# Performance work log

Measured on AMD Instinct MI355X. Metric: run time of the kernel, lower is better.

The kernel has to match this reference:

```python
import jax, jax.numpy as jnp
import numpy as np

NUM_CODES = 8192
CODE_DIM = 64
DECAY = 0.99
EPS = 1e-05


def setup_inputs() -> dict:
    key = jax.random.key(0)
    k1, k2 = jax.random.split(key)
    z = jax.random.normal(k1, (8, CODE_DIM, 64, 64), dtype=jnp.float32)
    embed = jax.random.normal(k2, (NUM_CODES, CODE_DIM), dtype=jnp.float32)
    embed = embed / jnp.linalg.norm(embed, axis=1, keepdims=True)  # F.normalize(dim=1)
    cluster_size = jnp.zeros((NUM_CODES,), dtype=jnp.float32)
    embed_avg = embed * 1.0
    return {"z": z, "embed": embed, "cluster_size": cluster_size, "embed_avg": embed_avg}


def reference(z, embed, cluster_size, embed_avg):
    B, C, H, W = z.shape
    # (B,C,H,W) -> (N, C), N = B*H*W
    flat = jnp.transpose(z, (0, 2, 3, 1)).reshape(-1, C)
    x2 = jnp.sum(flat * flat, axis=1, keepdims=True)
    e2 = jnp.sum(embed * embed, axis=1)[None, :]
    logits = x2 + e2 - 2.0 * (flat @ embed.T)
    codes = jnp.argmin(logits, axis=1)
    # gather nearest code vectors, restore (B,C,H,W)
    z_q = jnp.transpose(embed[codes].reshape(B, H, W, C), (0, 3, 1, 2))
    # EMA update (training path; equivalent to one-hot matmul via segment sums)
    cs_batch = jax.ops.segment_sum(jnp.ones_like(codes, dtype=flat.dtype), codes, num_segments=NUM_CODES)
    embed_sum = jax.ops.segment_sum(flat, codes, num_segments=NUM_CODES)
    new_cluster_size = cluster_size * DECAY + cs_batch * (1.0 - DECAY)
    new_embed_avg = embed_avg * DECAY + embed_sum * (1.0 - DECAY)
    n = jnp.sum(new_cluster_size)
    cs_smoothed = (new_cluster_size + EPS) / (n + NUM_CODES * EPS) * n
    new_embed = new_embed_avg / cs_smoothed[:, None]
    new_embed = new_embed / jnp.linalg.norm(new_embed, axis=1, keepdims=True)
    return z_q, codes.reshape(B, H, W), new_embed, new_cluster_size, new_embed_avg
```

## Files before the change

kernel.cpp:

```cpp
#include <hip/hip_runtime.h>
#include <math.h>
#include <float.h>

#define NPTS   32768
#define NCODES 8192
#define D      64
#define HWSZ   4096
#define KSPLIT 8
#define NSTAGE 16

#define DECAY_F 0.99f
#define OMD_F   ((float)(1.0 - 0.99))
#define EPS_F   1e-5f

typedef __attribute__((ext_vector_type(8)))  short bf16x8;
typedef __attribute__((ext_vector_type(8)))  unsigned short us8;
typedef __attribute__((ext_vector_type(4)))  float f32x4;
typedef __attribute__((ext_vector_type(16))) float f32x16;

#define ZQ_OFF    0
#define CODES_OFF 2097152
#define NE_OFF    2129920
#define NCS_OFF   2654208
#define NEA_OFF   2662400

#define WS_PSUM   0
#define WS_ME2    64
#define WS_HIST   8256
#define WS_BOFF   16448
#define WS_BOFF2  24640
#define WS_CODES  32832
#define WS_ORDER  65600
#define WS_PMG    98368
#define WS_EBI    1146944
#define WS_ZROW   1409088

__device__ __forceinline__ unsigned short f2bf(float x) {
    unsigned int u = __float_as_uint(x);
    unsigned int r = (u + 0x7fffu + ((u >> 16) & 1u)) >> 16;
    return (unsigned short)r;
}
__device__ __forceinline__ float bf2f(unsigned short b) {
    return __uint_as_float(((unsigned int)b) << 16);
}

__global__ __launch_bounds__(256) void k_prep_e(
    const float* __restrict__ embed,
    unsigned short* __restrict__ ebi,
    float* __restrict__ me2, int* __restrict__ hist)
{
    const int tid = threadIdx.x;
    const int c = blockIdx.x * 32 + (tid >> 3);
    const int s = tid & 7;
    const float4 v0 = *(const float4*)(embed + (size_t)c * D + s * 8);
    const float4 v1 = *(const float4*)(embed + (size_t)c * D + s * 8 + 4);
    float x[8] = {v0.x, v0.y, v0.z, v0.w, v1.x, v1.y, v1.z, v1.w};
    float s2 = 0.f;
#pragma unroll
    for (int j = 0; j < 8; ++j) s2 += x[j] * x[j];
    s2 += __shfl_xor(s2, 1);
    s2 += __shfl_xor(s2, 2);
    s2 += __shfl_xor(s2, 4);
    us8 p0, p1;
#pragma unroll
    for (int j = 0; j < 8; ++j) {
        unsigned short a = f2bf(x[j]);
        float r = x[j] - bf2f(a);
        p0[j] = a; p1[j] = f2bf(r);
    }
    const int sg = c >> 6, ci = c & 63;
    unsigned short* tile = ebi + (size_t)sg * 8192;
    *(us8*)(tile + s * 512 + ci * 8) = p0;
    *(us8*)(tile + 4096 + s * 512 + ci * 8) = p1;
    if (s == 0) {
        me2[c] = -0.5f * s2;
        hist[c] = 0;
    }
}

#define MFMA32 __builtin_amdgcn_mfma_f32_32x32x16_bf16

#define TOP2(nt, g, gi) { \
    bool c1 = (g) > b1m[nt]; \
    bool c2 = (g) > b2m[nt]; \
    b2m[nt] = c1 ? b1m[nt] : (c2 ? (g) : b2m[nt]); \
    b2g[nt] = c1 ? b1g[nt] : (c2 ? (gi) : b2g[nt]); \
    b1m[nt] = c1 ? (g) : b1m[nt]; \
    b1g[nt] = c1 ? (gi) : b1g[nt]; }

#define GMAX8(a, o) fmaxf(fmaxf(fmaxf(fmaxf(a[o+0], a[o+1]), a[o+2]), \
                                fmaxf(fmaxf(a[o+3], a[o+4]), a[o+5])), \
                          fmaxf(a[o+6], a[o+7]))

__global__ __launch_bounds__(256, 3) void k_argmin_mfma(
    const float* __restrict__ z,
    const unsigned short* __restrict__ ebi,
    float* __restrict__ pmg)
{
    __shared__ __align__(16) char ets[2 * 16384];

    const int tid = threadIdx.x;
    const int l = tid & 63;
    const int w = tid >> 6;
    const int l31 = l & 31;
    const int hi = l >> 5;
    const int split = blockIdx.x >> 7;
    const int pgrp  = blockIdx.x & 127;
    const int n0    = pgrp * 256;
    const int b     = n0 >> 12;
    const int hw0   = n0 & 4095;
    const int ptw   = n0 + w * 64;

    const char* ebase = (const char*)ebi;
#define ISSUE_STAGE(sg_, buf_) { \
    const char* gsrc_ = ebase + (size_t)(sg_) * 16384; \
    _Pragma("unroll") \
    for (int i_ = 0; i_ < 4; ++i_) { \
        __builtin_amdgcn_global_load_lds( \
            (const __attribute__((address_space(1))) void*)(gsrc_ + i_ * 4096 + w * 1024 + l * 16), \
            (__attribute__((address_space(3))) void*)(ets + (buf_) * 16384 + i_ * 4096 + w * 1024), \
            16, 0, 0); \
    } }

    ISSUE_STAGE(split * NSTAGE, 0)

    const float* zb = z + (size_t)b * D * HWSZ;
    us8 zf[2][2][4];
#pragma unroll
    for (int nt = 0; nt < 2; ++nt) {
        const int hwp = hw0 + w * 64 + nt * 32 + l31;
#pragma unroll
        for (int kc = 0; kc < 4; ++kc) {
            us8 p0, p1;
#pragma unroll
            for (int j = 0; j < 8; ++j) {
                float x = zb[(size_t)(kc * 16 + hi * 8 + j) * HWSZ + hwp];
                unsigned short a = f2bf(x);
                float r = x - bf2f(a);
                p0[j] = a; p1[j] = f2bf(r);
            }
            zf[nt][0][kc] = p0; zf[nt][1][kc] = p1;
        }
    }

    f32x16 zerov;
#pragma unroll
    for (int r = 0; r < 16; ++r) zerov[r] = 0.f;

    __syncthreads();

    float b1m[2] = {-FLT_MAX, -FLT_MAX}, b2m[2] = {-FLT_MAX, -FLT_MAX};
    int   b1g[2] = {0, 0},               b2g[2] = {0, 0};

    for (int stg = 0; stg < NSTAGE; ++stg) {
        const int sg = split * NSTAGE + stg;
        if (stg) {
            asm volatile("s_waitcnt vmcnt(0)" ::: "memory");
            __builtin_amdgcn_s_barrier();
            __builtin_amdgcn_sched_barrier(0);
        }
        if (stg + 1 < NSTAGE) ISSUE_STAGE(sg + 1, (stg + 1) & 1)

        const char* bt = ets + (stg & 1) * 16384;

        f32x16 accA0, accA1, accB0, accB1;
#pragma unroll
        for (int kc = 0; kc < 4; ++kc) {
            const size_t offc0 = (size_t)(kc * 2 + hi) * 1024 + (size_t)l31 * 16;
            const size_t offc1 = offc0 + 32 * 16;
            bf16x8 ea0c0 = *(const bf16x8*)(bt + offc0);
            bf16x8 ea1c0 = *(const bf16x8*)(bt + 8192 + offc0);
            bf16x8 ea0c1 = *(const bf16x8*)(bt + offc1);
            bf16x8 ea1c1 = *(const bf16x8*)(bt + 8192 + offc1);
            if (kc == 0) {
                accA0 = MFMA32(ea1c0, (bf16x8)zf[0][0][0], zerov, 0, 0, 0);
                accB0 = MFMA32(ea1c1, (bf16x8)zf[0][0][0], zerov, 0, 0, 0);
                accA1 = MFMA32(ea1c0, (bf16x8)zf[1][0][0], zerov, 0, 0, 0);
                accB1 = MFMA32(ea1c1, (bf16x8)zf[1][0][0], zerov, 0, 0, 0);
            } else {
                accA0 = MFMA32(ea1c0, (bf16x8)zf[0][0][kc], accA0, 0, 0, 0);
                accB0 = MFMA32(ea1c1, (bf16x8)zf[0][0][kc], accB0, 0, 0, 0);
                accA1 = MFMA32(ea1c0, (bf16x8)zf[1][0][kc], accA1, 0, 0, 0);
                accB1 = MFMA32(ea1c1, (bf16x8)zf[1][0][kc], accB1, 0, 0, 0);
            }
            accA0 = MFMA32(ea0c0, (bf16x8)zf[0][1][kc], accA0, 0, 0, 0);
            accB0 = MFMA32(ea0c1, (bf16x8)zf[0][1][kc], accB0, 0, 0, 0);
            accA1 = MFMA32(ea0c0, (bf16x8)zf[1][1][kc], accA1, 0, 0, 0);
            accB1 = MFMA32(ea0c1, (bf16x8)zf[1][1][kc], accB1, 0, 0, 0);
            accA0 = MFMA32(ea0c0, (bf16x8)zf[0][0][kc], accA0, 0, 0, 0);
            accB0 = MFMA32(ea0c1, (bf16x8)zf[0][0][kc], accB0, 0, 0, 0);
            accA1 = MFMA32(ea0c0, (bf16x8)zf[1][0][kc], accA1, 0, 0, 0);
            accB1 = MFMA32(ea0c1, (bf16x8)zf[1][0][kc], accB1, 0, 0, 0);
        }

        {
            const int gb0 = sg * 8 + hi;
            const int gb1 = sg * 8 + 4 + hi;
            float a00 = GMAX8(accA0, 0), a01 = GMAX8(accA0, 8);
            float a10 = GMAX8(accA1, 0), a11 = GMAX8(accA1, 8);
            float b00 = GMAX8(accB0, 0), b01 = GMAX8(accB0, 8);
            float b10 = GMAX8(accB1, 0), b11 = GMAX8(accB1, 8);
            TOP2(0, a00, gb0)
            TOP2(0, a01, gb0 + 2)
            TOP2(1, a10, gb0)
            TOP2(1, a11, gb0 + 2)
            TOP2(0, b00, gb1)
            TOP2(0, b01, gb1 + 2)
            TOP2(1, b10, gb1)
            TOP2(1, b11, gb1 + 2)
        }
    }

#pragma unroll
    for (int nt = 0; nt < 2; ++nt) {
        float o1 = __shfl_xor(b1m[nt], 32); int o1g = __shfl_xor(b1g[nt], 32);
        float o2 = __shfl_xor(b2m[nt], 32); int o2g = __shfl_xor(b2g[nt], 32);
        float n1m, n2m; int n1g, n2g;
        if (o1 > b1m[nt]) {
            n1m = o1; n1g = o1g;
            if (b1m[nt] >= o2) { n2m = b1m[nt]; n2g = b1g[nt]; } else { n2m = o2; n2g = o2g; }
        } else {
            n1m = b1m[nt]; n1g = b1g[nt];
            if (o1 >= b2m[nt]) { n2m = o1; n2g = o1g; } else { n2m = b2m[nt]; n2g = b2g[nt]; }
        }
        b1m[nt] = n1m; b1g[nt] = n1g; b2m[nt] = n2m; b2g[nt] = n2g;
    }
    if (l < 32) {
#pragma unroll
        for (int nt = 0; nt < 2; ++nt) {
            int pt = ptw + nt * 32 + l31;
            float4 v = {b1m[nt], __int_as_float(b1g[nt]), b2m[nt], __int_as_float(b2g[nt])};
            *(float4*)(pmg + ((size_t)split * NPTS + pt) * 4) = v;
        }
    }
}

__device__ __forceinline__ int grp_code(int g, int s) {
    int base = (g >> 3) * 64 + ((g >> 2) & 1) * 32 + ((g >> 1) & 1) * 16 + (g & 1) * 4;
    return base + (s & 3) + ((s >> 2) & 1) * 8;
}

__global__ __launch_bounds__(256) void k_refine(
    const float* __restrict__ z, const float* __restrict__ embed,
    const float* __restrict__ me2, const float* __restrict__ pmg,
    int* __restrict__ codes_i, float* __restrict__ out_codes,
    float* __restrict__ zq, int* __restrict__ hist, float* __restrict__ zrow)
{
    __shared__ float  xs[64 * 32];
    __shared__ float4 smg[256];
    __shared__ float  sbm[256];
    __shared__ int    sbi[256];
    const int tid = threadIdx.x;
    const int pi = tid & 31, s = tid >> 5;
    const int n0 = blockIdx.x * 32;
    const int b = n0 >> 12, hw0 = n0 & 4095;
    const int n = n0 + pi;

    {
        float4 v = ((const float4*)pmg)[(size_t)(tid & 7) * NPTS + n0 + (tid >> 3)];
        smg[(tid & 7) * 32 + (tid >> 3)] = v;
    }
    const float* zb = z + (size_t)b * D * HWSZ + hw0;
#pragma unroll
    for (int i = 0; i < 8; ++i) {
        int c = s * 8 + i;
        xs[c * 32 + pi] = zb[(size_t)c * HWSZ + pi];
    }
    __syncthreads();
    float x[64];
#pragma unroll
    for (int c = 0; c < 64; ++c) x[c] = xs[c * 32 + pi];

    float t1 = -FLT_MAX, t2 = -FLT_MAX; int g1 = 0, g2 = 0;
#pragma unroll
    for (int j = 0; j < 8; ++j) {
        float4 v = smg[j * 32 + pi];
        float m1 = v.x; int a1 = __float_as_int(v.y);
        float m2 = v.z; int a2 = __float_as_int(v.w);
        if (m1 > t1) { t2 = t1; g2 = g1; t1 = m1; g1 = a1; }
        else if (m1 > t2) { t2 = m1; g2 = a1; }
        if (m2 > t1) { t2 = t1; g2 = g1; t1 = m2; g1 = a2; }
        else if (m2 > t2) { t2 = m2; g2 = a2; }
    }

    float bm = -FLT_MAX; int bi = 0x7fffffff;
#pragma unroll
    for (int cset = 0; cset < 2; ++cset) {
        const int ci = grp_code(cset ? g2 : g1, s);
        const float4* er = (const float4*)(embed + (size_t)ci * D);
        float d0 = 0.f, d1 = 0.f, d2 = 0.f, d3 = 0.f;
#pragma unroll
        for (int q = 0; q < 16; ++q) {
            float4 e4 = er[q];
            d0 = fmaf(x[4 * q + 0], e4.x, d0);
            d1 = fmaf(x[4 * q + 1], e4.y, d1);
            d2 = fmaf(x[4 * q + 2], e4.z, d2);
            d3 = fmaf(x[4 * q + 3], e4.w, d3);
        }
        float m = ((d0 + d1) + (d2 + d3)) + me2[ci];
        if (m > bm || (m == bm && ci < bi)) { bm = m; bi = ci; }
    }
    sbm[tid] = bm; sbi[tid] = bi;
    __syncthreads();

    if (s == 0) {
        float B = sbm[pi]; int I = sbi[pi];
#pragma unroll
        for (int t = 1; t < 8; ++t) {
            float mm = sbm[t * 32 + pi]; int ii = sbi[t * 32 + pi];
            if (mm > B || (mm == B && ii < I)) { B = mm; I = ii; }
        }
        codes_i[n] = I;
        out_codes[n] = (float)I;
        atomicAdd(&hist[I], 1);
        sbi[pi] = I;
    }
    __syncthreads();
    {
        const int I = sbi[pi];
        const float* err = embed + (size_t)I * D;
        const float4 e0 = *(const float4*)(err + s * 8);
        const float4 e1 = *(const float4*)(err + s * 8 + 4);
        float ev[8] = {e0.x, e0.y, e0.z, e0.w, e1.x, e1.y, e1.z, e1.w};
        size_t zoff = (size_t)b * D * HWSZ + hw0 + pi;
#pragma unroll
        for (int j = 0; j < 8; ++j)
            zq[zoff + (size_t)(s * 8 + j) * HWSZ] = ev[j];
    }
    {
        float4 a4 = {x[s * 8 + 0], x[s * 8 + 1], x[s * 8 + 2], x[s * 8 + 3]};
        float4 b4 = {x[s * 8 + 4], x[s * 8 + 5], x[s * 8 + 6], x[s * 8 + 7]};
        *(float4*)(zrow + (size_t)n * 64 + s * 8) = a4;
        *(float4*)(zrow + (size_t)n * 64 + s * 8 + 4) = b4;
    }
}

__global__ __launch_bounds__(1024) void k_scan(
    const int* __restrict__ hist, const float* __restrict__ cs_in,
    int* __restrict__ binoff, int* __restrict__ binoff2, float* __restrict__ psum)
{
    __shared__ int wtot[16];
    __shared__ int wbase[16];
    __shared__ float csw[16];
    const int tid = threadIdx.x;
    const int lane = tid & 63, w = tid >> 6;
    int v[8]; int s = 0;
    float cz = 0.f;
#pragma unroll
    for (int i = 0; i < 8; ++i) {
        v[i] = hist[tid * 8 + i];
        s += v[i];
        cz += cs_in[tid * 8 + i];
    }
    int inc = s;
#pragma unroll
    for (int off = 1; off < 64; off <<= 1) {
        int t = __shfl_up(inc, off);
        if (lane >= off) inc += t;
    }
    cz += __shfl_xor(cz, 32); cz += __shfl_xor(cz, 16); cz += __shfl_xor(cz, 8);
    cz += __shfl_xor(cz, 4);  cz += __shfl_xor(cz, 2);  cz += __shfl_xor(cz, 1);
    if (lane == 63) wtot[w] = inc;
    if (lane == 0)  csw[w] = cz;
    __syncthreads();
    if (tid == 0) {
        int a = 0;
        float S = 0.f;
#pragma unroll
        for (int i = 0; i < 16; ++i) { int t = wtot[i]; wbase[i] = a; a += t; S += csw[i]; }
        psum[0] = S;
    }
    __syncthreads();
    int excl = wbase[w] + (inc - s);
#pragma unroll
    for (int i = 0; i < 8; ++i) {
        binoff[tid * 8 + i] = excl;
        binoff2[tid * 8 + i] = excl;
        excl += v[i];
    }
}

__global__ void k_reorder(const int* __restrict__ codes_i,
                          int* __restrict__ binoff2, int* __restrict__ order)
{
    int n = blockIdx.x * 256 + threadIdx.x;
    int c = codes_i[n];
    int r = atomicAdd(&binoff2[c], 1);
    order[r] = n;
}

__global__ __launch_bounds__(256) void k_accum(
    const int* __restrict__ hist, const int* __restrict__ binoff,
    const int* __restrict__ order, const float* __restrict__ zrow,
    const float* __restrict__ cs, const float* __restrict__ eavg,
    const float* __restrict__ psum,
    float* __restrict__ out_ncs, float* __restrict__ out_nea, float* __restrict__ out_ne)
{
    int k = blockIdx.x * 4 + (threadIdx.x >> 6);
    int lane = threadIdx.x & 63;
    int cnt = hist[k], base = binoff[k];
    float acc = 0.f;
    for (int i = 0; i < cnt; ++i) {
        int p = order[base + i];
        acc += zrow[(size_t)p * 64 + lane];
    }
    float S = psum[0];
    float n = DECAY_F * S + OMD_F * (float)NPTS;

    float v = cs[k] * DECAY_F + (float)cnt * OMD_F;
    if (lane == 0) out_ncs[k] = v;

    int idx = k * D + lane;
    float ea = eavg[idx] * DECAY_F + acc * OMD_F;
    out_nea[idx] = ea;
    float csm = (v + EPS_F) / (n + (float)NCODES * EPS_F) * n;
    float u = ea / csm;
    float ss = u * u;
    ss += __shfl_xor(ss, 32);
    ss += __shfl_xor(ss, 16);
    ss += __shfl_xor(ss, 8);
    ss += __shfl_xor(ss, 4);
    ss += __shfl_xor(ss, 2);
    ss += __shfl_xor(ss, 1);
    out_ne[idx] = u / sqrtf(ss);
}

extern "C" void kernel_launch(void* const* d_in, const int* in_sizes, int n_in,
                              void* d_out, int out_size, void* d_ws, size_t ws_size,
                              hipStream_t stream) {
    const float* z     = (const float*)d_in[0];
    const float* embed = (const float*)d_in[1];
    const float* cs    = (const float*)d_in[2];
    const float* eavg  = (const float*)d_in[3];

    float* out = (float*)d_out;
    float* zq        = out + ZQ_OFF;
    float* out_codes = out + CODES_OFF;
    float* out_ne    = out + NE_OFF;
    float* out_ncs   = out + NCS_OFF;
    float* out_nea   = out + NEA_OFF;

    float* ws = (float*)d_ws;
    float* psum   = ws + WS_PSUM;
    float* me2    = ws + WS_ME2;
    int*   hist   = (int*)(ws + WS_HIST);
    int*   boff   = (int*)(ws + WS_BOFF);
    int*   boff2  = (int*)(ws + WS_BOFF2);
    int*   codesi = (int*)(ws + WS_CODES);
    int*   order  = (int*)(ws + WS_ORDER);
    float* pmg    = ws + WS_PMG;
    float* zrow   = ws + WS_ZROW;
    unsigned short* ebi = (unsigned short*)(ws + WS_EBI);

    k_prep_e<<<NCODES / 32, 256, 0, stream>>>(embed, ebi, me2, hist);
    k_argmin_mfma<<<128 * KSPLIT, 256, 0, stream>>>(z, ebi, pmg);
    k_refine<<<NPTS / 32, 256, 0, stream>>>(z, embed, me2, pmg,
                                            codesi, out_codes, zq, hist, zrow);
    k_scan<<<1, 1024, 0, stream>>>(hist, cs, boff, boff2, psum);
    k_reorder<<<NPTS / 256, 256, 0, stream>>>(codesi, boff2, order);
    k_accum<<<NCODES / 4, 256, 0, stream>>>(hist, boff, order, zrow, cs, eavg, psum,
                                            out_ncs, out_nea, out_ne);
}
```

Baseline: 135.8 us.

## Fuse scan into refine via last-block counter and widen refine to 512 threads

The separate single-block scan kernel is removed. Its prefix sum over the histogram and its cluster-size sum now run in whichever refine block finishes last, detected with a global atomic counter that the prep kernel resets. The refine kernel also doubles to 512 threads, so each thread scores one candidate code instead of two and reads x from shared memory instead of a 64-register array. This saves one launch and cuts register pressure, at the cost of a serialized tail in the last block and reliance on threadfence/atomic ordering for the histogram.

```diff
diff --git a/kernel.cpp b/kernel.cpp
--- a/kernel.cpp
+++ b/kernel.cpp
@@ -47,7 +47,7 @@
 __global__ __launch_bounds__(256) void k_prep_e(
     const float* __restrict__ embed,
     unsigned short* __restrict__ ebi,
-    float* __restrict__ me2, int* __restrict__ hist)
+    float* __restrict__ me2, int* __restrict__ hist, int* __restrict__ rctr)
 {
     const int tid = threadIdx.x;
     const int c = blockIdx.x * 32 + (tid >> 3);
@@ -76,6 +76,7 @@
         me2[c] = -0.5f * s2;
         hist[c] = 0;
     }
+    if (blockIdx.x == 0 && tid == 0) rctr[0] = 0;
 }
 
 #define MFMA32 __builtin_amdgcn_mfma_f32_32x32x16_bf16
@@ -235,41 +236,42 @@
     }
 }
 
-__device__ __forceinline__ int grp_code(int g, int s) {
+__device__ __forceinline__ int grp_code(int g, int j) {
     int base = (g >> 3) * 64 + ((g >> 2) & 1) * 32 + ((g >> 1) & 1) * 16 + (g & 1) * 4;
-    return base + (s & 3) + ((s >> 2) & 1) * 8;
-}
-
-__global__ __launch_bounds__(256) void k_refine(
+    return base + (j & 3) + ((j >> 2) & 1) * 8;
+}
+
+__global__ __launch_bounds__(512) void k_refine(
     const float* __restrict__ z, const float* __restrict__ embed,
     const float* __restrict__ me2, const float* __restrict__ pmg,
+    const float* __restrict__ cs_in,
     int* __restrict__ codes_i, float* __restrict__ out_codes,
-    float* __restrict__ zq, int* __restrict__ hist, float* __restrict__ zrow)
+    float* __restrict__ zq, int* __restrict__ hist, float* __restrict__ zrow,
+    int* __restrict__ rctr, int* __restrict__ binoff, int* __restrict__ binoff2,
+    float* __restrict__ psum)
 {
     __shared__ float  xs[64 * 32];
     __shared__ float4 smg[256];
-    __shared__ float  sbm[256];
-    __shared__ int    sbi[256];
+    __shared__ float  sbm[512];
+    __shared__ int    sbi[512];
+    __shared__ int    lastflag;
     const int tid = threadIdx.x;
     const int pi = tid & 31, s = tid >> 5;
     const int n0 = blockIdx.x * 32;
     const int b = n0 >> 12, hw0 = n0 & 4095;
     const int n = n0 + pi;
 
-    {
+    if (tid < 256) {
         float4 v = ((const float4*)pmg)[(size_t)(tid & 7) * NPTS + n0 + (tid >> 3)];
         smg[(tid & 7) * 32 + (tid >> 3)] = v;
     }
     const float* zb = z + (size_t)b * D * HWSZ + hw0;
 #pragma unroll
-    for (int i = 0; i < 8; ++i) {
-        int c = s * 8 + i;
+    for (int i = 0; i < 4; ++i) {
+        int c = s * 4 + i;
         xs[c * 32 + pi] = zb[(size_t)c * HWSZ + pi];
     }
     __syncthreads();
-    float x[64];
-#pragma unroll
-    for (int c = 0; c < 64; ++c) x[c] = xs[c * 32 + pi];
 
     float t1 = -FLT_MAX, t2 = -FLT_MAX; int g1 = 0, g2 = 0;
 #pragma unroll
@@ -283,30 +285,29 @@
         else if (m2 > t2) { t2 = m2; g2 = a2; }
     }
 
-    float bm = -FLT_MAX; int bi = 0x7fffffff;
-#pragma unroll
-    for (int cset = 0; cset < 2; ++cset) {
-        const int ci = grp_code(cset ? g2 : g1, s);
+    const int ci = grp_code((s < 8) ? g1 : g2, s & 7);
+    float4 e[16];
+    {
         const float4* er = (const float4*)(embed + (size_t)ci * D);
-        float d0 = 0.f, d1 = 0.f, d2 = 0.f, d3 = 0.f;
-#pragma unroll
-        for (int q = 0; q < 16; ++q) {
-            float4 e4 = er[q];
-            d0 = fmaf(x[4 * q + 0], e4.x, d0);
-            d1 = fmaf(x[4 * q + 1], e4.y, d1);
-            d2 = fmaf(x[4 * q + 2], e4.z, d2);
-            d3 = fmaf(x[4 * q + 3], e4.w, d3);
-        }
-        float m = ((d0 + d1) + (d2 + d3)) + me2[ci];
-        if (m > bm || (m == bm && ci < bi)) { bm = m; bi = ci; }
-    }
-    sbm[tid] = bm; sbi[tid] = bi;
+#pragma unroll
+        for (int q = 0; q < 16; ++q) e[q] = er[q];
+    }
+    float d0 = 0.f, d1 = 0.f, d2 = 0.f, d3 = 0.f;
+#pragma unroll
+    for (int q = 0; q < 16; ++q) {
+        d0 = fmaf(xs[(4 * q + 0) * 32 + pi], e[q].x, d0);
+        d1 = fmaf(xs[(4 * q + 1) * 32 + pi], e[q].y, d1);
+        d2 = fmaf(xs[(4 * q + 2) * 32 + pi], e[q].z, d2);
+        d3 = fmaf(xs[(4 * q + 3) * 32 + pi], e[q].w, d3);
+    }
+    float m = ((d0 + d1) + (d2 + d3)) + me2[ci];
+    sbm[tid] = m; sbi[tid] = ci;
     __syncthreads();
 
     if (s == 0) {
         float B = sbm[pi]; int I = sbi[pi];
 #pragma unroll
-        for (int t = 1; t < 8; ++t) {
+        for (int t = 1; t < 16; ++t) {
             float mm = sbm[t * 32 + pi]; int ii = sbi[t * 32 + pi];
             if (mm > B || (mm == B && ii < I)) { B = mm; I = ii; }
         }
@@ -318,65 +319,70 @@
     __syncthreads();
     {
         const int I = sbi[pi];
-        const float* err = embed + (size_t)I * D;
-        const float4 e0 = *(const float4*)(err + s * 8);
-        const float4 e1 = *(const float4*)(err + s * 8 + 4);
-        float ev[8] = {e0.x, e0.y, e0.z, e0.w, e1.x, e1.y, e1.z, e1.w};
+        const float4 ev = *(const float4*)(embed + (size_t)I * D + s * 4);
         size_t zoff = (size_t)b * D * HWSZ + hw0 + pi;
-#pragma unroll
-        for (int j = 0; j < 8; ++j)
-            zq[zoff + (size_t)(s * 8 + j) * HWSZ] = ev[j];
-    }
-    {
-        float4 a4 = {x[s * 8 + 0], x[s * 8 + 1], x[s * 8 + 2], x[s * 8 + 3]};
-        float4 b4 = {x[s * 8 + 4], x[s * 8 + 5], x[s * 8 + 6], x[s * 8 + 7]};
+        zq[zoff + (size_t)(s * 4 + 0) * HWSZ] = ev.x;
+        zq[zoff + (size_t)(s * 4 + 1) * HWSZ] = ev.y;
+        zq[zoff + (size_t)(s * 4 + 2) * HWSZ] = ev.z;
+        zq[zoff + (size_t)(s * 4 + 3) * HWSZ] = ev.w;
+    }
+    if (s < 8) {
+        float4 a4 = {xs[(s * 8 + 0) * 32 + pi], xs[(s * 8 + 1) * 32 + pi],
+                     xs[(s * 8 + 2) * 32 + pi], xs[(s * 8 + 3) * 32 + pi]};
+        float4 b4 = {xs[(s * 8 + 4) * 32 + pi], xs[(s * 8 + 5) * 32 + pi],
+                     xs[(s * 8 + 6) * 32 + pi], xs[(s * 8 + 7) * 32 + pi]};
         *(float4*)(zrow + (size_t)n * 64 + s * 8) = a4;
         *(float4*)(zrow + (size_t)n * 64 + s * 8 + 4) = b4;
     }
-}
-
-__global__ __launch_bounds__(1024) void k_scan(
-    const int* __restrict__ hist, const float* __restrict__ cs_in,
-    int* __restrict__ binoff, int* __restrict__ binoff2, float* __restrict__ psum)
-{
-    __shared__ int wtot[16];
-    __shared__ int wbase[16];
-    __shared__ float csw[16];
-    const int tid = threadIdx.x;
-    const int lane = tid & 63, w = tid >> 6;
-    int v[8]; int s = 0;
-    float cz = 0.f;
-#pragma unroll
-    for (int i = 0; i < 8; ++i) {
-        v[i] = hist[tid * 8 + i];
-        s += v[i];
-        cz += cs_in[tid * 8 + i];
-    }
-    int inc = s;
-#pragma unroll
-    for (int off = 1; off < 64; off <<= 1) {
-        int t = __shfl_up(inc, off);
-        if (lane >= off) inc += t;
-    }
-    cz += __shfl_xor(cz, 32); cz += __shfl_xor(cz, 16); cz += __shfl_xor(cz, 8);
-    cz += __shfl_xor(cz, 4);  cz += __shfl_xor(cz, 2);  cz += __shfl_xor(cz, 1);
-    if (lane == 63) wtot[w] = inc;
-    if (lane == 0)  csw[w] = cz;
+
     __syncthreads();
     if (tid == 0) {
-        int a = 0;
-        float S = 0.f;
-#pragma unroll
-        for (int i = 0; i < 16; ++i) { int t = wtot[i]; wbase[i] = a; a += t; S += csw[i]; }
-        psum[0] = S;
-    }
-    __syncthreads();
-    int excl = wbase[w] + (inc - s);
-#pragma unroll
-    for (int i = 0; i < 8; ++i) {
-        binoff[tid * 8 + i] = excl;
-        binoff2[tid * 8 + i] = excl;
-        excl += v[i];
+        __threadfence();
+        int d = atomicAdd(rctr, 1);
+        lastflag = (d == (int)gridDim.x - 1);
+    }
+    __syncthreads();
+    if (!lastflag) return;
+
+    {
+        __shared__ int wtot[8];
+        __shared__ int wbase[8];
+        __shared__ float csw[8];
+        const int lane = tid & 63, w = tid >> 6;
+        int v[16]; int ssum = 0;
+        float cz = 0.f;
+#pragma unroll
+        for (int i = 0; i < 16; ++i) {
+            v[i] = hist[tid * 16 + i];
+            ssum += v[i];
+            cz += cs_in[tid * 16 + i];
+        }
+        int inc = ssum;
+#pragma unroll
+        for (int off = 1; off < 64; off <<= 1) {
+            int t = __shfl_up(inc, off);
+            if (lane >= off) inc += t;
+        }
+        cz += __shfl_xor(cz, 32); cz += __shfl_xor(cz, 16); cz += __shfl_xor(cz, 8);
+        cz += __shfl_xor(cz, 4);  cz += __shfl_xor(cz, 2);  cz += __shfl_xor(cz, 1);
+        if (lane == 63) wtot[w] = inc;
+        if (lane == 0)  csw[w] = cz;
+        __syncthreads();
+        if (tid == 0) {
+            int a = 0;
+            float S = 0.f;
+#pragma unroll
+            for (int i = 0; i < 8; ++i) { int t = wtot[i]; wbase[i] = a; a += t; S += csw[i]; }
+            psum[0] = S;
+        }
+        __syncthreads();
+        int excl = wbase[w] + (inc - ssum);
+#pragma unroll
+        for (int i = 0; i < 16; ++i) {
+            binoff[tid * 16 + i] = excl;
+            binoff2[tid * 16 + i] = excl;
+            excl += v[i];
+        }
     }
 }
 
@@ -442,6 +448,7 @@
 
     float* ws = (float*)d_ws;
     float* psum   = ws + WS_PSUM;
+    int*   rctr   = (int*)(ws + WS_PSUM + 8);
     float* me2    = ws + WS_ME2;
     int*   hist   = (int*)(ws + WS_HIST);
     int*   boff   = (int*)(ws + WS_BOFF);
@@ -452,11 +459,11 @@
     float* zrow   = ws + WS_ZROW;
     unsigned short* ebi = (unsigned short*)(ws + WS_EBI);
 
-    k_prep_e<<<NCODES / 32, 256, 0, stream>>>(embed, ebi, me2, hist);
+    k_prep_e<<<NCODES / 32, 256, 0, stream>>>(embed, ebi, me2, hist, rctr);
     k_argmin_mfma<<<128 * KSPLIT, 256, 0, stream>>>(z, ebi, pmg);
-    k_refine<<<NPTS / 32, 256, 0, stream>>>(z, embed, me2, pmg,
-                                            codesi, out_codes, zq, hist, zrow);
-    k_scan<<<1, 1024, 0, stream>>>(hist, cs, boff, boff2, psum);
+    k_refine<<<NPTS / 32, 512, 0, stream>>>(z, embed, me2, pmg, cs,
+                                            codesi, out_codes, zq, hist, zrow,
+                                            rctr, boff, boff2, psum);
     k_reorder<<<NPTS / 256, 256, 0, stream>>>(codesi, boff2, order);
     k_accum<<<NCODES / 4, 256, 0, stream>>>(hist, boff, order, zrow, cs, eavg, psum,
                                             out_ncs, out_nea, out_ne);
```

Result: slower. 162.2 us (+19.5%).
